# Performance work log

Measured on AMD Instinct MI355X. Metric: run time of the kernel, lower is better.

Reference implementation:

```python
import jax, jax.numpy as jnp
import numpy as np

B, H, N, D = 2, 16, 2048, 64

def setup_inputs() -> dict:
    key = jax.random.key(0)
    ks = jax.random.split(key, 5)
    q = jax.random.normal(ks[0], (B, H, N, D), dtype=jnp.float32)
    k = jax.random.normal(ks[1], (B, H, N, D), dtype=jnp.float32)
    v = jax.random.normal(ks[2], (B, H, N, D), dtype=jnp.float32)
    # 1x1 Conv2d(heads, heads, bias=False) == HxH linear mixing over the head dim
    W_pre = jax.random.normal(ks[3], (H, H), dtype=jnp.float32) * (1.0 / jnp.sqrt(H))
    W_post = jax.random.normal(ks[4], (H, H), dtype=jnp.float32) * (1.0 / jnp.sqrt(H))
    return {"q": q, "k": k, "v": v, "W_pre": W_pre, "W_post": W_post}

def reference(q, k, v, W_pre, W_post):
    heads = q.shape[1]
    d_head = q.shape[-1]
    # original: scale = (1/sqrt(heads)) / sqrt(d_head)
    scale = 1.0 / (jnp.sqrt(jnp.float32(heads)) * jnp.sqrt(jnp.float32(d_head)))
    # pre-softmax talking heads applied to BOTH q and k (head-mixing linear)
    q = jnp.einsum('ef,bfnd->bend', W_pre, q)
    k = jnp.einsum('ef,bfnd->bend', W_pre, k)
    attn_weights = jnp.einsum('bhid,bhjd->bhij', q, k) * scale  # [B,H,N,N]
    i = q.shape[-2]
    j = k.shape[-2]
    causal_mask = jnp.triu(jnp.ones((i, j), dtype=bool), k=1)
    attn_weights = jnp.where(causal_mask, -jnp.inf, attn_weights)
    # softmax computed in float32 (dtype=torch.float32 in attn_fn)
    attn_probs = jax.nn.softmax(attn_weights.astype(jnp.float32), axis=-1)
    # dropout p=0.0 -> identity
    attn_probs = jnp.einsum('ef,bfij->beij', W_post, attn_probs)
    attn_output = jnp.einsum('bhij,bhjd->bhid', attn_probs, v)
    return attn_output
```

## Files before the change

### kernel.cpp

```cpp
#include <hip/hip_runtime.h>
#include <math.h>

typedef _Float16 Hh;
typedef __attribute__((ext_vector_type(8))) _Float16 half8;
typedef __attribute__((ext_vector_type(4))) _Float16 half4;
typedef __attribute__((ext_vector_type(4))) float float4v;

#define B_ 2
#define H_ 16
#define N_ 2048
#define D_ 64
#define ND_ (N_*D_)
#define C1 0.04508422f

#define EB_JS 324
#define EB_IS 20
#define PM_ES 580
#define PM_IS 36

__global__ __launch_bounds__(256) void prep_kernel(const float* __restrict__ q,
    const float* __restrict__ k, const float* __restrict__ v,
    const float* __restrict__ Wpre,
    Hh* __restrict__ qb, Hh* __restrict__ kb, Hh* __restrict__ vt2)
{
    int tid = threadIdx.x;
    int bid = blockIdx.x;
    if (bid < 512) {
        __shared__ float wsh[256];
        wsh[tid] = Wpre[tid];
        __syncthreads();
        int tensor = bid >> 8;
        int g = ((bid & 255) << 8) | tid;
        int b = g >> 15;
        int r = g & 32767;
        const float4* src = (const float4*)(tensor ? k : q);
        Hh* dst = tensor ? kb : qb;
        float4 x[16];
        #pragma unroll
        for (int f=0; f<16; f++) x[f] = src[(size_t)(b*16+f)*32768 + r];
        #pragma unroll
        for (int e=0; e<16; e++) {
            float4 a = make_float4(0.f,0.f,0.f,0.f);
            #pragma unroll
            for (int f=0; f<16; f++) {
                float wv = wsh[e*16+f];
                a.x += wv*x[f].x; a.y += wv*x[f].y; a.z += wv*x[f].z; a.w += wv*x[f].w;
            }
            half4 hv; hv[0]=(Hh)a.x; hv[1]=(Hh)a.y; hv[2]=(Hh)a.z; hv[3]=(Hh)a.w;
            *(half4*)(dst + (size_t)(b*16+e)*ND_ + (size_t)r*4) = hv;
        }
    } else {
        __shared__ Hh tile[64*48];
        int tb = bid - 512;
        int be = tb >> 3;
        int jtg = tb & 7;
        const float4* v4 = (const float4*)v;
        for (int u=0; u<8; u++) {
            int jt = jtg*8 + u;
            #pragma unroll
            for (int p=0; p<2; p++) {
                int j = p*16 + (tid>>4);
                int d4 = tid & 15;
                float4 val = v4[(size_t)be*32768 + (size_t)(jt*32+j)*16 + d4];
                tile[(d4*4+0)*48 + j] = (Hh)val.x;
                tile[(d4*4+1)*48 + j] = (Hh)val.y;
                tile[(d4*4+2)*48 + j] = (Hh)val.z;
                tile[(d4*4+3)*48 + j] = (Hh)val.w;
            }
            __syncthreads();
            {
                int d = tid >> 2;
                int jc = (tid & 3) * 8;
                half8 o;
                #pragma unroll
                for (int z=0; z<8; z++) o[z] = tile[d*48 + jc + z];
                *(half8*)(vt2 + ((size_t)(be*64) + jt)*2048 + (size_t)tid*8) = o;
            }
            __syncthreads();
        }
    }
}

__global__ __launch_bounds__(512) void denom_kernel(const Hh* __restrict__ qb,
    const Hh* __restrict__ kb, float* __restrict__ lacc_g)
{
    int bid = blockIdx.x;
    int s = bid & 7;
    int idx = 127 - (bid >> 3);
    int b = idx & 1, it = idx >> 1;
    if (s > it) return;

    int i0 = it * 32;
    int tid = threadIdx.x;
    int lane = tid & 63, w = tid >> 6;
    int qd = lane >> 4, c = lane & 15;
    int f0 = 2*w;

    half8 aq[2][2][2];
    #pragma unroll
    for (int fi=0; fi<2; fi++) {
        #pragma unroll
        for (int ig=0; ig<2; ig++) {
            const Hh* qr = qb + (size_t)((b*16+f0+fi)*N_ + i0 + ig*16 + c)*64 + qd*8;
            aq[fi][ig][0] = *(const half8*)qr;
            aq[fi][ig][1] = *(const half8*)(qr+32);
        }
    }
    float lacc[2][2][4];
    #pragma unroll
    for (int fi=0;fi<2;fi++) for (int ig=0;ig<2;ig++) for (int r=0;r<4;r++) lacc[fi][ig][r]=0.f;

    for (int jt = s; jt <= it; jt += 8) {
        int j0 = jt*32;
        #pragma unroll
        for (int fi=0; fi<2; fi++) {
            #pragma unroll
            for (int jh=0; jh<2; jh++) {
                const Hh* kr = kb + (size_t)((b*16+f0+fi)*N_ + j0 + jh*16 + c)*64 + qd*8;
                half8 b0 = *(const half8*)kr;
                half8 b1 = *(const half8*)(kr+32);
                #pragma unroll
                for (int ig=0; ig<2; ig++) {
                    float4v sv = {0.f,0.f,0.f,0.f};
                    sv = __builtin_amdgcn_mfma_f32_16x16x32_f16(aq[fi][ig][0], b0, sv, 0,0,0);
                    sv = __builtin_amdgcn_mfma_f32_16x16x32_f16(aq[fi][ig][1], b1, sv, 0,0,0);
                    #pragma unroll
                    for (int r=0; r<4; r++) {
                        int i = i0 + ig*16 + qd*4 + r;
                        int j = j0 + jh*16 + c;
                        float ev = (j <= i) ? __builtin_amdgcn_exp2f(sv[r]*C1) : 0.f;
                        lacc[fi][ig][r] += ev;
                    }
                }
            }
        }
    }
    #pragma unroll
    for (int fi=0; fi<2; fi++) {
        #pragma unroll
        for (int ig=0; ig<2; ig++) {
            #pragma unroll
            for (int r=0; r<4; r++) {
                float vs = lacc[fi][ig][r];
                vs += __shfl_xor(vs, 1);
                vs += __shfl_xor(vs, 2);
                vs += __shfl_xor(vs, 4);
                vs += __shfl_xor(vs, 8);
                if (c == 0)
                    unsafeAtomicAdd(&lacc_g[(size_t)(b*16+f0+fi)*N_ + i0 + ig*16 + qd*4 + r], vs);
            }
        }
    }
}

__global__ __launch_bounds__(512,4) void attend_kernel(const Hh* __restrict__ qb,
    const Hh* __restrict__ kb, const Hh* __restrict__ vt2,
    const float* __restrict__ lacc_g, const float* __restrict__ Wpost,
    float* __restrict__ out)
{
    __shared__ Hh Ebuf[32*EB_JS];
    __shared__ Hh Pm[16*PM_ES];

    int bid = blockIdx.x;
    int s = bid & 3;
    int idx = 255 - (bid >> 2);
    int b = idx & 1, it = idx >> 1;
    int jtmax = it >> 1;
    if (s > jtmax) return;
    int i0 = it * 16;

    int tid = threadIdx.x;
    int lane = tid & 63, w = tid >> 6;
    int qd = lane >> 4, c = lane & 15;

    int fg = w & 3, jh = w >> 2;
    half8 aq[4][2];
    float lgr[4][4];
    #pragma unroll
    for (int ff=0; ff<4; ff++) {
        int f = 4*fg + ff;
        const Hh* qr = qb + (size_t)((b*16+f)*N_ + i0 + c)*64 + qd*8;
        aq[ff][0] = *(const half8*)qr;
        aq[ff][1] = *(const half8*)(qr+32);
        #pragma unroll
        for (int r=0; r<4; r++)
            lgr[ff][r] = __builtin_amdgcn_logf(
                lacc_g[(size_t)(b*16+f)*N_ + i0 + qd*4 + r]);
    }
    int jh2 = w & 1, ib = 4*(w>>1);
    half4 wf;
    #pragma unroll
    for (int z=0; z<4; z++) wf[z] = (Hh)Wpost[c*16 + qd*4 + z];

    float4v acc[2][4];
    #pragma unroll
    for (int el=0; el<2; el++) for (int nc=0; nc<4; nc++)
        acc[el][nc] = (float4v){0.f,0.f,0.f,0.f};

    auto scores = [&](int jt) {
        int jc = jt*32 + jh*16;
        float4v sv[4];
        #pragma unroll
        for (int ff=0; ff<4; ff++) {
            int f = 4*fg + ff;
            const Hh* kr = kb + (size_t)((b*16+f)*N_ + jc + c)*64 + qd*8;
            half8 b0 = *(const half8*)kr;
            half8 b1 = *(const half8*)(kr+32);
            float4v t = {0.f,0.f,0.f,0.f};
            t = __builtin_amdgcn_mfma_f32_16x16x32_f16(aq[ff][0], b0, t, 0,0,0);
            t = __builtin_amdgcn_mfma_f32_16x16x32_f16(aq[ff][1], b1, t, 0,0,0);
            sv[ff] = t;
        }
        int j = jc + c;
        #pragma unroll
        for (int r=0; r<4; r++) {
            int i = i0 + qd*4 + r;
            half4 h;
            #pragma unroll
            for (int ff=0; ff<4; ff++)
                h[ff] = (Hh)((j <= i) ? __builtin_amdgcn_exp2f(sv[ff][r]*C1 - lgr[ff][r]) : 0.f);
            *(half4*)&Ebuf[(jh*16+c)*EB_JS + (qd*4+r)*EB_IS + fg*4] = h;
        }
    };

    scores(s);
    __syncthreads();

    for (int jt = s; jt <= jtmax; jt += 4) {
        #pragma unroll
        for (int ii=0; ii<4; ii++) {
            int i = ib + ii;
            half4 ef = *(const half4*)&Ebuf[(jh2*16+c)*EB_JS + i*EB_IS + qd*4];
            float4v cc = {0.f,0.f,0.f,0.f};
            cc = __builtin_amdgcn_mfma_f32_16x16x16f16(ef, wf, cc, 0,0,0);
            half4 hv;
            #pragma unroll
            for (int r=0; r<4; r++) hv[r] = (Hh)cc[r];
            *(half4*)&Pm[c*PM_ES + i*PM_IS + jh2*16 + qd*4] = hv;
        }
        __syncthreads();
        #pragma unroll
        for (int el=0; el<2; el++) {
            int e = 2*w + el;
            half8 pa = *(const half8*)&Pm[e*PM_ES + c*PM_IS + qd*8];
            #pragma unroll
            for (int nc=0; nc<4; nc++) {
                const Hh* vr = vt2 + (size_t)((b*16+e)*64 + jt)*2048 + (nc*16+c)*32 + qd*8;
                half8 vb = *(const half8*)vr;
                acc[el][nc] = __builtin_amdgcn_mfma_f32_16x16x32_f16(pa, vb, acc[el][nc], 0,0,0);
            }
        }
        if (jt + 4 <= jtmax) scores(jt + 4);
        __syncthreads();
    }

    #pragma unroll
    for (int el=0; el<2; el++) {
        int e = 2*w + el;
        #pragma unroll
        for (int nc=0; nc<4; nc++) {
            #pragma unroll
            for (int r=0; r<4; r++)
                unsafeAtomicAdd(&out[(size_t)((b*16+e)*N_ + i0 + qd*4 + r)*64 + nc*16 + c],
                                acc[el][nc][r]);
        }
    }
}

extern "C" void kernel_launch(void* const* d_in, const int* in_sizes, int n_in,
                              void* d_out, int out_size, void* d_ws, size_t ws_size,
                              hipStream_t stream) {
    const float* q     = (const float*)d_in[0];
    const float* k     = (const float*)d_in[1];
    const float* v     = (const float*)d_in[2];
    const float* Wpre  = (const float*)d_in[3];
    const float* Wpost = (const float*)d_in[4];
    float* out = (float*)d_out;

    size_t tsz = (size_t)B_*H_*N_*D_;
    Hh* qb = (Hh*)d_ws;
    Hh* kb = qb + tsz;
    Hh* vt2 = kb + tsz;
    float* lacc = (float*)(vt2 + tsz);

    hipMemsetAsync(lacc, 0, (size_t)B_*H_*N_*sizeof(float), stream);
    hipMemsetAsync(out, 0, (size_t)out_size*sizeof(float), stream);
    prep_kernel<<<768, 256, 0, stream>>>(q, k, v, Wpre, qb, kb, vt2);
    denom_kernel<<<1024, 512, 0, stream>>>(qb, kb, lacc);
    attend_kernel<<<1024, 512, 0, stream>>>(qb, kb, vt2, lacc, Wpost, out);
}
```

Before: 268.6 us.

## Double query-row tile sizes in denom and attend kernels to reuse K/V loads

The denominator kernel now handles 64 query rows per block instead of 32, and the attend kernel handles 32 rows instead of 16, with grids halved to match. Each loaded K tile and V tile now serves twice as many query rows, which cuts global/L2 traffic per unit of work. In exchange each thread holds more registers (the attend kernel's occupancy hint drops from 4 to 2 blocks per CU), LDS buffers roughly double, and there are fewer blocks, so latency hiding and load balance across the causal triangle get worse.

```diff
diff --git a/kernel.cpp b/kernel.cpp
--- a/kernel.cpp
+++ b/kernel.cpp
@@ -13,9 +13,9 @@
 #define ND_ (N_*D_)
 #define C1 0.04508422f
 
-#define EB_JS 324
+#define EB_JS 644
 #define EB_IS 20
-#define PM_ES 580
+#define PM_ES 1156
 #define PM_IS 36
 
 __global__ __launch_bounds__(256) void prep_kernel(const float* __restrict__ q,
@@ -86,31 +86,32 @@
 {
     int bid = blockIdx.x;
     int s = bid & 7;
-    int idx = 127 - (bid >> 3);
+    int idx = 63 - (bid >> 3);
     int b = idx & 1, it = idx >> 1;
-    if (s > it) return;
-
-    int i0 = it * 32;
+    int jtmax = 2*it + 1;
+    if (s > jtmax) return;
+    int i0 = it * 64;
+
     int tid = threadIdx.x;
     int lane = tid & 63, w = tid >> 6;
     int qd = lane >> 4, c = lane & 15;
     int f0 = 2*w;
 
-    half8 aq[2][2][2];
+    half8 aq[2][4][2];
     #pragma unroll
     for (int fi=0; fi<2; fi++) {
         #pragma unroll
-        for (int ig=0; ig<2; ig++) {
+        for (int ig=0; ig<4; ig++) {
             const Hh* qr = qb + (size_t)((b*16+f0+fi)*N_ + i0 + ig*16 + c)*64 + qd*8;
             aq[fi][ig][0] = *(const half8*)qr;
             aq[fi][ig][1] = *(const half8*)(qr+32);
         }
     }
-    float lacc[2][2][4];
-    #pragma unroll
-    for (int fi=0;fi<2;fi++) for (int ig=0;ig<2;ig++) for (int r=0;r<4;r++) lacc[fi][ig][r]=0.f;
-
-    for (int jt = s; jt <= it; jt += 8) {
+    float lacc[2][4][4];
+    #pragma unroll
+    for (int fi=0;fi<2;fi++) for (int ig=0;ig<4;ig++) for (int r=0;r<4;r++) lacc[fi][ig][r]=0.f;
+
+    for (int jt = s; jt <= jtmax; jt += 8) {
         int j0 = jt*32;
         #pragma unroll
         for (int fi=0; fi<2; fi++) {
@@ -120,7 +121,7 @@
                 half8 b0 = *(const half8*)kr;
                 half8 b1 = *(const half8*)(kr+32);
                 #pragma unroll
-                for (int ig=0; ig<2; ig++) {
+                for (int ig=0; ig<4; ig++) {
                     float4v sv = {0.f,0.f,0.f,0.f};
                     sv = __builtin_amdgcn_mfma_f32_16x16x32_f16(aq[fi][ig][0], b0, sv, 0,0,0);
                     sv = __builtin_amdgcn_mfma_f32_16x16x32_f16(aq[fi][ig][1], b1, sv, 0,0,0);
@@ -138,7 +139,7 @@
     #pragma unroll
     for (int fi=0; fi<2; fi++) {
         #pragma unroll
-        for (int ig=0; ig<2; ig++) {
+        for (int ig=0; ig<4; ig++) {
             #pragma unroll
             for (int r=0; r<4; r++) {
                 float vs = lacc[fi][ig][r];
@@ -153,7 +154,7 @@
     }
 }
 
-__global__ __launch_bounds__(512,4) void attend_kernel(const Hh* __restrict__ qb,
+__global__ __launch_bounds__(512,2) void attend_kernel(const Hh* __restrict__ qb,
     const Hh* __restrict__ kb, const Hh* __restrict__ vt2,
     const float* __restrict__ lacc_g, const float* __restrict__ Wpost,
     float* __restrict__ out)
@@ -163,63 +164,76 @@
 
     int bid = blockIdx.x;
     int s = bid & 3;
-    int idx = 255 - (bid >> 2);
+    int idx = 127 - (bid >> 2);
     int b = idx & 1, it = idx >> 1;
-    int jtmax = it >> 1;
-    if (s > jtmax) return;
-    int i0 = it * 16;
+    if (s > it) return;
+    int i0 = it * 32;
+    int jtmax = it;
 
     int tid = threadIdx.x;
     int lane = tid & 63, w = tid >> 6;
     int qd = lane >> 4, c = lane & 15;
-
-    int fg = w & 3, jh = w >> 2;
+    int ig = w >> 2;
+    int fg = w & 3;
+    int fb = fg * 4;
+
     half8 aq[4][2];
     float lgr[4][4];
     #pragma unroll
     for (int ff=0; ff<4; ff++) {
-        int f = 4*fg + ff;
-        const Hh* qr = qb + (size_t)((b*16+f)*N_ + i0 + c)*64 + qd*8;
+        int f = fb + ff;
+        const Hh* qr = qb + (size_t)((b*16+f)*N_ + i0 + ig*16 + c)*64 + qd*8;
         aq[ff][0] = *(const half8*)qr;
         aq[ff][1] = *(const half8*)(qr+32);
         #pragma unroll
         for (int r=0; r<4; r++)
             lgr[ff][r] = __builtin_amdgcn_logf(
-                lacc_g[(size_t)(b*16+f)*N_ + i0 + qd*4 + r]);
-    }
-    int jh2 = w & 1, ib = 4*(w>>1);
+                lacc_g[(size_t)(b*16+f)*N_ + i0 + ig*16 + qd*4 + r]);
+    }
     half4 wf;
     #pragma unroll
     for (int z=0; z<4; z++) wf[z] = (Hh)Wpost[c*16 + qd*4 + z];
 
-    float4v acc[2][4];
-    #pragma unroll
-    for (int el=0; el<2; el++) for (int nc=0; nc<4; nc++)
+    float4v acc[4][4];
+    #pragma unroll
+    for (int el=0; el<4; el++) for (int nc=0; nc<4; nc++)
         acc[el][nc] = (float4v){0.f,0.f,0.f,0.f};
 
     auto scores = [&](int jt) {
-        int jc = jt*32 + jh*16;
-        float4v sv[4];
+        int j0 = jt*32;
+        half8 kr0[4][2], kr1[4][2];
         #pragma unroll
         for (int ff=0; ff<4; ff++) {
-            int f = 4*fg + ff;
-            const Hh* kr = kb + (size_t)((b*16+f)*N_ + jc + c)*64 + qd*8;
-            half8 b0 = *(const half8*)kr;
-            half8 b1 = *(const half8*)(kr+32);
-            float4v t = {0.f,0.f,0.f,0.f};
-            t = __builtin_amdgcn_mfma_f32_16x16x32_f16(aq[ff][0], b0, t, 0,0,0);
-            t = __builtin_amdgcn_mfma_f32_16x16x32_f16(aq[ff][1], b1, t, 0,0,0);
-            sv[ff] = t;
-        }
-        int j = jc + c;
-        #pragma unroll
-        for (int r=0; r<4; r++) {
-            int i = i0 + qd*4 + r;
-            half4 h;
-            #pragma unroll
-            for (int ff=0; ff<4; ff++)
-                h[ff] = (Hh)((j <= i) ? __builtin_amdgcn_exp2f(sv[ff][r]*C1 - lgr[ff][r]) : 0.f);
-            *(half4*)&Ebuf[(jh*16+c)*EB_JS + (qd*4+r)*EB_IS + fg*4] = h;
+            #pragma unroll
+            for (int jh=0; jh<2; jh++) {
+                const Hh* kr = kb + (size_t)((b*16+fb+ff)*N_ + j0 + jh*16 + c)*64 + qd*8;
+                kr0[ff][jh] = *(const half8*)kr;
+                kr1[ff][jh] = *(const half8*)(kr+32);
+            }
+        }
+        float4v sv[4][2];
+        #pragma unroll
+        for (int ff=0; ff<4; ff++) {
+            #pragma unroll
+            for (int jh=0; jh<2; jh++) {
+                float4v t = {0.f,0.f,0.f,0.f};
+                t = __builtin_amdgcn_mfma_f32_16x16x32_f16(aq[ff][0], kr0[ff][jh], t, 0,0,0);
+                t = __builtin_amdgcn_mfma_f32_16x16x32_f16(aq[ff][1], kr1[ff][jh], t, 0,0,0);
+                sv[ff][jh] = t;
+            }
+        }
+        #pragma unroll
+        for (int jh=0; jh<2; jh++) {
+            #pragma unroll
+            for (int r=0; r<4; r++) {
+                int i = i0 + ig*16 + qd*4 + r;
+                int j = j0 + jh*16 + c;
+                half4 h;
+                #pragma unroll
+                for (int ff=0; ff<4; ff++)
+                    h[ff] = (Hh)((j <= i) ? __builtin_amdgcn_exp2f(sv[ff][jh][r]*C1 - lgr[ff][r]) : 0.f);
+                *(half4*)&Ebuf[(jh*16+c)*EB_JS + (ig*16+qd*4+r)*EB_IS + fb] = h;
+            }
         }
     };
 
@@ -228,21 +242,24 @@
 
     for (int jt = s; jt <= jtmax; jt += 4) {
         #pragma unroll
-        for (int ii=0; ii<4; ii++) {
-            int i = ib + ii;
-            half4 ef = *(const half4*)&Ebuf[(jh2*16+c)*EB_JS + i*EB_IS + qd*4];
-            float4v cc = {0.f,0.f,0.f,0.f};
-            cc = __builtin_amdgcn_mfma_f32_16x16x16f16(ef, wf, cc, 0,0,0);
-            half4 hv;
-            #pragma unroll
-            for (int r=0; r<4; r++) hv[r] = (Hh)cc[r];
-            *(half4*)&Pm[c*PM_ES + i*PM_IS + jh2*16 + qd*4] = hv;
+        for (int jh2=0; jh2<2; jh2++) {
+            #pragma unroll
+            for (int ii=0; ii<4; ii++) {
+                int i = 4*w + ii;
+                half4 ef = *(const half4*)&Ebuf[(jh2*16+c)*EB_JS + i*EB_IS + qd*4];
+                float4v cc = {0.f,0.f,0.f,0.f};
+                cc = __builtin_amdgcn_mfma_f32_16x16x16f16(ef, wf, cc, 0,0,0);
+                half4 hv;
+                #pragma unroll
+                for (int r=0; r<4; r++) hv[r] = (Hh)cc[r];
+                *(half4*)&Pm[c*PM_ES + i*PM_IS + jh2*16 + qd*4] = hv;
+            }
         }
         __syncthreads();
         #pragma unroll
-        for (int el=0; el<2; el++) {
-            int e = 2*w + el;
-            half8 pa = *(const half8*)&Pm[e*PM_ES + c*PM_IS + qd*8];
+        for (int el=0; el<4; el++) {
+            int e = fg*4 + el;
+            half8 pa = *(const half8*)&Pm[e*PM_ES + (ig*16+c)*PM_IS + qd*8];
             #pragma unroll
             for (int nc=0; nc<4; nc++) {
                 const Hh* vr = vt2 + (size_t)((b*16+e)*64 + jt)*2048 + (nc*16+c)*32 + qd*8;
@@ -255,13 +272,13 @@
     }
 
     #pragma unroll
-    for (int el=0; el<2; el++) {
-        int e = 2*w + el;
+    for (int el=0; el<4; el++) {
+        int e = fg*4 + el;
         #pragma unroll
         for (int nc=0; nc<4; nc++) {
             #pragma unroll
             for (int r=0; r<4; r++)
-                unsafeAtomicAdd(&out[(size_t)((b*16+e)*N_ + i0 + qd*4 + r)*64 + nc*16 + c],
+                unsafeAtomicAdd(&out[(size_t)((b*16+e)*N_ + i0 + ig*16 + qd*4 + r)*64 + nc*16 + c],
                                 acc[el][nc][r]);
         }
     }
@@ -286,6 +303,6 @@
     hipMemsetAsync(lacc, 0, (size_t)B_*H_*N_*sizeof(float), stream);
     hipMemsetAsync(out, 0, (size_t)out_size*sizeof(float), stream);
     prep_kernel<<<768, 256, 0, stream>>>(q, k, v, Wpre, qb, kb, vt2);
-    denom_kernel<<<1024, 512, 0, stream>>>(qb, kb, lacc);
-    attend_kernel<<<1024, 512, 0, stream>>>(qb, kb, vt2, lacc, Wpost, out);
+    denom_kernel<<<512, 512, 0, stream>>>(qb, kb, lacc);
+    attend_kernel<<<512, 512, 0, stream>>>(qb, kb, vt2, lacc, Wpost, out);
 }
```

New measurement: 314.2 us. +17.0%, slower.
